# Kernel tuning notes

Hardware: AMD Instinct MI355X
Metric: run time of the kernel (lower is better)

Reference implementation:

```python
import jax, jax.numpy as jnp
import numpy as np

N_NODES = 100_000
M_EDGES = 500_000
F = 128       # elem_fea_len
H = 3         # elem_heads
HD = 256      # hidden layer dim of gate/message nets
BN_EPS = 1e-5


def setup_inputs() -> dict:
    key = jax.random.key(0)
    ks = jax.random.split(key, 12)
    s = 0.05
    return {
        "elem_weights": jax.random.uniform(ks[0], (N_NODES, 1), jnp.float32, 0.05, 1.0),
        "elem_in_fea": jax.random.normal(ks[1], (N_NODES, F), jnp.float32),
        "gate_W1": jax.random.normal(ks[2], (H, 2 * F, HD), jnp.float32) * s,
        "gate_b1": jnp.zeros((H, HD), jnp.float32),
        "gate_g": jnp.ones((H, HD), jnp.float32),
        "gate_beta": jnp.zeros((H, HD), jnp.float32),
        "gate_Wo": jax.random.normal(ks[3], (H, HD, 1), jnp.float32) * s,
        "gate_bo": jnp.zeros((H, 1), jnp.float32),
        "msg_W1": jax.random.normal(ks[4], (H, 2 * F, HD), jnp.float32) * s,
        "msg_b1": jnp.zeros((H, HD), jnp.float32),
        "msg_g": jnp.ones((H, HD), jnp.float32),
        "msg_beta": jnp.zeros((H, HD), jnp.float32),
        "msg_Wo": jax.random.normal(ks[5], (H, HD, F), jnp.float32) * s,
        "msg_bo": jnp.zeros((H, F), jnp.float32),
        "pow_p": jax.random.normal(ks[6], (H, 1), jnp.float32),
        "self_fea_idx": jax.random.randint(ks[7], (M_EDGES,), 0, N_NODES, jnp.int32),
        "nbr_fea_idx": jax.random.randint(ks[8], (M_EDGES,), 0, N_NODES, jnp.int32),
    }


def _simple_net(x, W1, b1, g, beta, Wo, bo):
    # Linear -> BatchNorm1d (training-mode batch stats) -> SiLU -> Linear
    h = x @ W1 + b1
    mu = jnp.mean(h, axis=0)
    var = jnp.mean(jnp.square(h - mu), axis=0)  # biased var, as torch BN
    h = (h - mu) * jax.lax.rsqrt(var + BN_EPS) * g + beta
    h = jax.nn.silu(h)
    return h @ Wo + bo


def reference(elem_weights, elem_in_fea, gate_W1, gate_b1, gate_g, gate_beta,
              gate_Wo, gate_bo, msg_W1, msg_b1, msg_g, msg_beta, msg_Wo,
              msg_bo, pow_p, self_fea_idx, nbr_fea_idx):
    n = elem_in_fea.shape[0]
    # gather edge endpoint features: (M, 2F)
    fea = jnp.concatenate([elem_in_fea[self_fea_idx], elem_in_fea[nbr_fea_idx]], axis=1)
    w = elem_weights[nbr_fea_idx]  # (M, 1)

    def head(gW1, gb1, gg, gbe, gWo, gbo, mW1, mb1, mg, mbe, mWo, mbo, p):
        gate = _simple_net(fea, gW1, gb1, gg, gbe, gWo, gbo)          # (M, 1)
        gmax = jax.ops.segment_max(gate, self_fea_idx, num_segments=n)
        gate = (w ** p) * jnp.exp(gate - gmax[self_fea_idx])
        den = jax.ops.segment_sum(gate, self_fea_idx, num_segments=n)
        gate = gate / (den[self_fea_idx] + 1e-10)
        msg = _simple_net(fea, mW1, mb1, mg, mbe, mWo, mbo)           # (M, F)
        return jax.ops.segment_sum(gate * msg, self_fea_idx, num_segments=n)

    head_out = jax.vmap(head)(gate_W1, gate_b1, gate_g, gate_beta, gate_Wo,
                              gate_bo, msg_W1, msg_b1, msg_g, msg_beta,
                              msg_Wo, msg_bo, pow_p)                  # (H, N, F)
    return jnp.mean(head_out, axis=0) + elem_in_fea
```

## Files before the change

kernel.cpp:

```cpp
#include <hip/hip_runtime.h>
#include <stdint.h>

#define NN 100000
#define MM 500000
#define FD 128
#define KK 256
#define NHEADS 3
#define NTILES 3907

typedef __attribute__((ext_vector_type(8))) __bf16 bf16x8;
typedef __attribute__((ext_vector_type(4))) float floatx4;

__device__ __forceinline__ float bf2f(unsigned short u) {
    union { uint32_t i; float f; } c; c.i = ((uint32_t)u) << 16; return c.f;
}
__device__ __forceinline__ unsigned short f2bf(float f) {
    union { float f; uint32_t i; } c; c.f = f;
    uint32_t i = c.i;
    return (unsigned short)((i + 0x7FFFu + ((i >> 16) & 1u)) >> 16);
}
__device__ __forceinline__ unsigned short f2bf_hw(float f) {
    __bf16 h = (__bf16)f;
    return __builtin_bit_cast(unsigned short, h);
}
__device__ __forceinline__ float silu(float a) {
    float e = __expf(-a);
    return a * __builtin_amdgcn_rcpf(1.f + e);
}
__device__ __forceinline__ float silu_div(float a) { return a / (1.f + __expf(-a)); }
__device__ __forceinline__ float fin(float v) {
    return (v == v && fabsf(v) < 1e30f) ? v : 0.f;
}
__device__ __forceinline__ void gl_lds16(const void* g, void* l) {
    __builtin_amdgcn_global_load_lds(
        (const __attribute__((address_space(1))) unsigned int*)g,
        (__attribute__((address_space(3))) unsigned int*)l, 16, 0, 0);
}
__device__ __forceinline__ void vm_drain() {
    asm volatile("s_waitcnt vmcnt(0)" ::: "memory");
}
__device__ __forceinline__ int swz_bid(int d, int nwg) {
    int qq = nwg >> 3, rr = nwg & 7;
    int xcd = d & 7, idx = d >> 3;
    int base = (xcd < rr) ? xcd * (qq + 1) : rr * (qq + 1) + (xcd - rr) * qq;
    return base + idx;
}

__global__ void k_zero(float* __restrict__ p, int nwords) {
    int i = blockIdx.x * 256 + threadIdx.x;
    if (i < nwords) p[i] = 0.f;
}

__global__ void k_castx(const float* __restrict__ x, unsigned short* __restrict__ xb) {
    int i = blockIdx.x * 256 + threadIdx.x;
    if (i < NN * FD / 2) {
        float2 v = ((const float2*)x)[i];
        uint32_t p = (uint32_t)f2bf(v.x) | ((uint32_t)f2bf(v.y) << 16);
        ((uint32_t*)xb)[i] = p;
    }
}

__global__ void k_transpose_w1(const float* __restrict__ gw1,
                               const float* __restrict__ mw1,
                               unsigned short* __restrict__ W1t) {
    int idx = blockIdx.x * 256 + threadIdx.x;
    int j = idx >> 16;
    int rem = idx & 65535;
    int n = rem >> 8, k = rem & 255;
    const float* src = (j < 3) ? (gw1 + (size_t)j * 65536)
                               : (mw1 + (size_t)(j - 3) * 65536);
    W1t[(size_t)idx] = f2bf(src[k * 256 + n]);
}
__global__ void k_transpose_wo(const float* __restrict__ mwo,
                               unsigned short* __restrict__ Wot) {
    int idx = blockIdx.x * 256 + threadIdx.x;
    int h = idx / 32768;
    int rem = idx % 32768;
    int f = rem >> 8, k = rem & 255;
    Wot[idx] = f2bf(mwo[(size_t)h * 32768 + k * 128 + f]);
}

__global__ void k_hist(const int* __restrict__ idx, int* __restrict__ cnt) {
    int e = blockIdx.x * 256 + threadIdx.x;
    if (e < MM) atomicAdd(&cnt[idx[e]], 1);
}
__global__ void k_scan1(const int* __restrict__ cnt, int* __restrict__ pincl, int* __restrict__ bsum) {
    __shared__ int s[256];
    int t = threadIdx.x;
    int i = blockIdx.x * 256 + t;
    int v = (i < NN) ? cnt[i] : 0;
    s[t] = v; __syncthreads();
    for (int o = 1; o < 256; o <<= 1) {
        int add = (t >= o) ? s[t - o] : 0;
        __syncthreads();
        s[t] += add;
        __syncthreads();
    }
    if (i < NN) pincl[i] = s[t];
    if (t == 255) bsum[blockIdx.x] = s[255];
}
__global__ void k_scan2(const int* __restrict__ bsum, int* __restrict__ boff, int nb) {
    __shared__ int s[512];
    int t = threadIdx.x;
    int v = (t < nb) ? bsum[t] : 0;
    s[t] = v; __syncthreads();
    for (int o = 1; o < 512; o <<= 1) {
        int add = (t >= o) ? s[t - o] : 0;
        __syncthreads();
        s[t] += add;
        __syncthreads();
    }
    if (t < nb) boff[t] = s[t] - v;
}
__global__ void k_scan3(const int* __restrict__ pincl, const int* __restrict__ boff, int* __restrict__ rp) {
    int i = blockIdx.x * 256 + threadIdx.x;
    if (i < NN) rp[i + 1] = pincl[i] + boff[i >> 8];
    if (i == 0) rp[0] = 0;
}
__global__ void k_scatter(const int* __restrict__ self, const int* __restrict__ rp,
                          int* __restrict__ fill, int* __restrict__ elist) {
    int e = blockIdx.x * 256 + threadIdx.x;
    if (e < MM) {
        int n = self[e];
        int pos = atomicAdd(&fill[n], 1);
        elist[rp[n] + pos] = e;
    }
}
__global__ void k_perm(const int* __restrict__ elist, const int* __restrict__ self,
                       const int* __restrict__ nbr, int* __restrict__ selfp, int* __restrict__ nbrp) {
    int i = blockIdx.x * 256 + threadIdx.x;
    if (i < MM) {
        int e = elist[i];
        selfp[i] = self[e];
        nbrp[i] = nbr[e];
    }
}

__global__ void k_colsum(const float* __restrict__ x,
                         const int* __restrict__ cnt_self, const int* __restrict__ cnt_nbr,
                         float* __restrict__ colsum) {
    int t = threadIdx.x;
    int col = t & 127, part = t >> 7;
    const int* cp = part ? cnt_nbr : cnt_self;
    int n0 = blockIdx.x * 512;
    float a = 0.f;
    for (int i = 0; i < 512; i++) {
        int n = n0 + i;
        if (n < NN) {
            float c = (float)cp[n];
            a += c * x[(size_t)n * FD + col];
        }
    }
    atomicAdd(&colsum[part * 128 + col], a);
}

#define NCH 7813
#define CPB 62
__global__ __launch_bounds__(256, 2)
void k_S(const unsigned short* __restrict__ xb,
         const int* __restrict__ self_idx, const int* __restrict__ nbr_idx,
         float* __restrict__ S) {
    __shared__ unsigned short LT[256][72];
    const int tid = threadIdx.x;
    const int e_l = tid & 63;
    const int half = tid >> 6;
    const int ti = blockIdx.y >> 1, tj = blockIdx.y & 1;
    const int lane = tid & 63, w = tid >> 6;
    const int lr = lane & 15, q = lane >> 4;

    int cbeg = blockIdx.x * CPB;
    int cend = cbeg + CPB; if (cend > NCH) cend = NCH;

    floatx4 acc[2][8];
#pragma unroll
    for (int a = 0; a < 2; a++)
#pragma unroll
        for (int b = 0; b < 8; b++)
#pragma unroll
            for (int r = 0; r < 4; r++) acc[a][b][r] = 0.f;

    for (int ch = cbeg; ch < cend; ch++) {
        int e = ch * 64 + e_l;
        union { uint4 v[8]; unsigned short us[64]; } buf;
        if (e < MM) {
            int node = (half < 2) ? self_idx[e] : nbr_idx[e];
            const unsigned short* src = xb + (size_t)node * FD + (half & 1) * 64;
#pragma unroll
            for (int u2 = 0; u2 < 8; u2++) buf.v[u2] = *(const uint4*)(src + u2 * 8);
        } else {
#pragma unroll
            for (int u2 = 0; u2 < 8; u2++) { buf.v[u2].x = 0u; buf.v[u2].y = 0u; buf.v[u2].z = 0u; buf.v[u2].w = 0u; }
        }
        __syncthreads();
#pragma unroll
        for (int j2 = 0; j2 < 64; j2++)
            LT[half * 64 + j2][e_l] = buf.us[j2];
        __syncthreads();
#pragma unroll
        for (int ks = 0; ks < 64; ks += 32) {
            bf16x8 aF[2], bF[8];
#pragma unroll
            for (int mi = 0; mi < 2; mi++)
                aF[mi] = *(const bf16x8*)&LT[ti * 128 + w * 32 + mi * 16 + lr][ks + q * 8];
#pragma unroll
            for (int nj = 0; nj < 8; nj++)
                bF[nj] = *(const bf16x8*)&LT[tj * 128 + nj * 16 + lr][ks + q * 8];
#pragma unroll
            for (int mi = 0; mi < 2; mi++)
#pragma unroll
                for (int nj = 0; nj < 8; nj++)
                    acc[mi][nj] = __builtin_amdgcn_mfma_f32_16x16x32_bf16(aF[mi], bF[nj], acc[mi][nj], 0, 0, 0);
        }
    }
#pragma unroll
    for (int mi = 0; mi < 2; mi++)
#pragma unroll
        for (int nj = 0; nj < 8; nj++)
#pragma unroll
            for (int r = 0; r < 4; r++) {
                int row = ti * 128 + w * 32 + mi * 16 + q * 4 + r;
                int col = tj * 128 + nj * 16 + lr;
                atomicAdd(&S[row * 256 + col], acc[mi][nj][r]);
            }
}

__global__ void k_stats(const float* __restrict__ S, const float* __restrict__ colsum,
                        const unsigned short* __restrict__ W1t,
                        const float* __restrict__ gg, const float* __restrict__ gbe,
                        const float* __restrict__ mg, const float* __restrict__ mbe,
                        float* __restrict__ scaleA, float* __restrict__ shiftA) {
    __shared__ float ws[16][257];
    __shared__ float qq[16], uu[16];
    int t = threadIdx.x;
    int j = blockIdx.y;
    int c0 = blockIdx.x * 16;
    const unsigned short* Wn = W1t + (size_t)j * 65536;
    const float* g    = (j < 3) ? gg + j * 256 : mg + (j - 3) * 256;
    const float* beta = (j < 3) ? gbe + j * 256 : mbe + (j - 3) * 256;
#pragma unroll
    for (int i = 0; i < 16; i++) ws[i][t] = bf2f(Wn[(size_t)(c0 + i) * 256 + t]);
    if (t < 16) { qq[t] = 0.f; uu[t] = 0.f; }
    __syncthreads();
    float vpart[16];
#pragma unroll
    for (int i = 0; i < 16; i++) vpart[i] = 0.f;
    for (int k = 0; k < 256; k++) {
        float s = S[k * 256 + t];
#pragma unroll
        for (int i = 0; i < 16; i++) vpart[i] += s * ws[i][k];
    }
    float cs = colsum[t];
    int lane = t & 63;
#pragma unroll
    for (int i = 0; i < 16; i++) {
        float q1 = ws[i][t] * vpart[i];
        float u1 = cs * ws[i][t];
#pragma unroll
        for (int m = 1; m <= 32; m <<= 1) { q1 += __shfl_xor(q1, m); u1 += __shfl_xor(u1, m); }
        if (lane == 0) { atomicAdd(&qq[i], q1); atomicAdd(&uu[i], u1); }
    }
    __syncthreads();
    if (t < 16) {
        int c = c0 + t;
        float mu = fin(uu[t] / (float)MM);
        float var = fmaxf(fin(qq[t] / (float)MM - mu * mu), 0.f);
        float sc = fin(g[c] * rsqrtf(var + 1e-5f));
        scaleA[j * 256 + c] = sc;
        shiftA[j * 256 + c] = fin(beta[c] - mu * sc);
    }
}

__global__ __launch_bounds__(256, 2)
void k_gate(const unsigned short* __restrict__ x,
            const int* __restrict__ selfp, const int* __restrict__ nbrp,
            const unsigned short* __restrict__ W1t,
            const float* __restrict__ scale, const float* __restrict__ shift,
            const float* __restrict__ wo, const float* __restrict__ bo,
            float* __restrict__ glog) {
    __shared__ unsigned char Bs[2][16384];
    __shared__ float sc[3][256], sh[3][256], wv[3][256];
    __shared__ int nid[128], nidN[128];

    const int tid = threadIdx.x;
    const int m0 = swz_bid(blockIdx.x, NTILES) * 128;
#pragma unroll
    for (int h = 0; h < 3; h++) {
        sc[h][tid] = scale[h * 256 + tid];
        sh[h][tid] = shift[h * 256 + tid];
        wv[h][tid] = wo[h * 256 + tid];
    }
    if (tid < 128) {
        int e = m0 + tid;
        nid[tid]  = (e < MM) ? selfp[e] : 0;
        nidN[tid] = (e < MM) ? nbrp[e] : 0;
    }
    __syncthreads();

    const int lane = tid & 63, w = tid >> 6;
    const int lr = lane & 15, q = lane >> 4;
    const int swz = (lr & 7) << 4;

    bf16x8 aReg[2][8];
    {
        const unsigned short* bS0 = x + (size_t)nid[w * 32 + lr] * FD;
        const unsigned short* bS1 = x + (size_t)nid[w * 32 + 16 + lr] * FD;
        const unsigned short* bN0 = x + (size_t)nidN[w * 32 + lr] * FD;
        const unsigned short* bN1 = x + (size_t)nidN[w * 32 + 16 + lr] * FD;
#pragma unroll
        for (int s = 0; s < 8; s++) {
            int koff = (s & 3) * 32 + q * 8;
            aReg[0][s] = *(const bf16x8*)(((s < 4) ? bS0 : bN0) + koff);
            aReg[1][s] = *(const bf16x8*)(((s < 4) ? bS1 : bN1) + koff);
        }
    }

    uint32_t pre[4];
#pragma unroll
    for (int c = 0; c < 4; c++) {
        int o = (w * 4 + c) * 1024 + lane * 16;
        int r = o >> 7, lc = o & 127;
        pre[c] = (uint32_t)(r * 512 + (lc ^ ((r & 7) << 4)));
    }

    auto STAGE = [&](int t, int b) {
        int hh = t >> 3, rr = t & 7, nh2 = rr >> 2, kc = rr & 3;
        const char* gb = (const char*)(W1t + (size_t)hh * 65536 + (size_t)nh2 * 32768 + kc * 64);
#pragma unroll
        for (int c = 0; c < 4; c++)
            gl_lds16(gb + pre[c], &Bs[b][(w * 4 + c) * 1024]);
    };

    STAGE(0, 0);
    vm_drain();
    __syncthreads();

    int buf = 0, tcur = 0;
    for (int h = 0; h < 3; h++) {
        float dotp[2][4];
#pragma unroll
        for (int mi = 0; mi < 2; mi++)
#pragma unroll
            for (int r = 0; r < 4; r++) dotp[mi][r] = 0.f;

        for (int nh = 0; nh < 2; nh++) {
            floatx4 acc[2][8];
#pragma unroll
            for (int a = 0; a < 2; a++)
#pragma unroll
                for (int b = 0; b < 8; b++)
#pragma unroll
                    for (int r = 0; r < 4; r++) acc[a][b][r] = 0.f;

#pragma unroll
            for (int kc = 0; kc < 4; kc++) {
                if (tcur + 1 < 24) STAGE(tcur + 1, buf ^ 1);
#pragma unroll
                for (int ks = 0; ks < 2; ks++) {
                    bf16x8 bF[8];
#pragma unroll
                    for (int nj = 0; nj < 8; nj++)
                        bF[nj] = *(const bf16x8*)&Bs[buf][(nj * 16 + lr) * 128 + ((ks * 64 + q * 16) ^ swz)];
                    __builtin_amdgcn_s_setprio(1);
#pragma unroll
                    for (int mi = 0; mi < 2; mi++)
#pragma unroll
                        for (int nj = 0; nj < 8; nj++)
                            acc[mi][nj] = __builtin_amdgcn_mfma_f32_16x16x32_bf16(aReg[mi][kc * 2 + ks], bF[nj], acc[mi][nj], 0, 0, 0);
                    __builtin_amdgcn_s_setprio(0);
                }
                vm_drain();
                __syncthreads();
                buf ^= 1; tcur++;
            }
#pragma unroll
            for (int mi = 0; mi < 2; mi++)
#pragma unroll
                for (int r = 0; r < 4; r++) {
                    float d = 0.f;
#pragma unroll
                    for (int nj = 0; nj < 8; nj++) {
                        int cg = nh * 128 + nj * 16 + lr;
                        float v = acc[mi][nj][r] * sc[h][cg] + sh[h][cg];
                        d += silu(v) * wv[h][cg];
                    }
                    dotp[mi][r] += d;
                }
        }
        float b0 = bo[h];
#pragma unroll
        for (int mi = 0; mi < 2; mi++)
#pragma unroll
            for (int r = 0; r < 4; r++) {
                float v = dotp[mi][r];
                v += __shfl_xor(v, 1); v += __shfl_xor(v, 2);
                v += __shfl_xor(v, 4); v += __shfl_xor(v, 8);
                if (lr == 0) {
                    int row = w * 32 + mi * 16 + q * 4 + r;
                    int e = m0 + row;
                    if (e < MM) glog[(size_t)h * MM + e] = fin(v + b0);
                }
            }
    }
}

__global__ void k_coef(const int* __restrict__ rp, const float* __restrict__ glog,
                       float* __restrict__ coef, const float* __restrict__ ew,
                       const int* __restrict__ nbrp, const float* __restrict__ powp) {
    int n = blockIdx.x * 256 + threadIdx.x;
    if (n >= NN) return;
    int b = rp[n], e = rp[n + 1];
    if (e <= b) return;
    int h = blockIdx.y;
    const float* gl = glog + (size_t)h * MM;
    float* cf = coef + (size_t)h * MM;
    float p = powp[h];
    float gmax = -3.4e38f;
    for (int i = b; i < e; i++) gmax = fmaxf(gmax, gl[i]);
    float den = 0.f;
    for (int i = b; i < e; i++) {
        float wvv = ew[nbrp[i]];
        float u = fin(powf(wvv, p) * __expf(gl[i] - gmax));
        cf[i] = u; den += u;
    }
    float inv = fin(1.f / (den + 1e-10f));
    for (int i = b; i < e; i++) cf[i] = fin(cf[i] * inv);
}

__global__ __launch_bounds__(256, 2)
void k_msg(const unsigned short* __restrict__ x,
           const int* __restrict__ selfp, const int* __restrict__ nbrp,
           const unsigned short* __restrict__ W1t,
           const float* __restrict__ scale, const float* __restrict__ shift,
           const unsigned short* __restrict__ Wo2t,
           const float* __restrict__ bo2,
           const float* __restrict__ coef,
           float* __restrict__ out_acc) {
    __shared__ unsigned char Bs[2][16384];
    __shared__ unsigned short ActC[128][72];
    __shared__ float sc[3][256], sh[3][256];
    __shared__ float bvec[3][128], cfs[3][128];
    __shared__ int nid[128], nidN[128];

    const int tid = threadIdx.x;
    const int m0 = blockIdx.x * 128;
#pragma unroll
    for (int h = 0; h < 3; h++) {
        sc[h][tid] = scale[h * 256 + tid];
        sh[h][tid] = shift[h * 256 + tid];
    }
    if (tid < 128) {
        int e = m0 + tid;
        nid[tid]  = (e < MM) ? selfp[e] : -1;
        nidN[tid] = (e < MM) ? nbrp[e] : 0;
#pragma unroll
        for (int h = 0; h < 3; h++) {
            bvec[h][tid] = bo2[h * 128 + tid];
            cfs[h][tid] = (e < MM) ? coef[(size_t)h * MM + e] : 0.f;
        }
    }
    __syncthreads();

    const int lane = tid & 63, w = tid >> 6;
    const int lr = lane & 15, q = lane >> 4;
    const int swz = (lr & 7) << 4;

    bf16x8 aReg[2][8];
    {
        int nS0 = nid[w * 32 + lr];      if (nS0 < 0) nS0 = 0;
        int nS1 = nid[w * 32 + 16 + lr]; if (nS1 < 0) nS1 = 0;
        const unsigned short* bS0 = x + (size_t)nS0 * FD;
        const unsigned short* bS1 = x + (size_t)nS1 * FD;
        const unsigned short* bN0 = x + (size_t)nidN[w * 32 + lr] * FD;
        const unsigned short* bN1 = x + (size_t)nidN[w * 32 + 16 + lr] * FD;
#pragma unroll
        for (int s = 0; s < 8; s++) {
            int koff = (s & 3) * 32 + q * 8;
            aReg[0][s] = *(const bf16x8*)(((s < 4) ? bS0 : bN0) + koff);
            aReg[1][s] = *(const bf16x8*)(((s < 4) ? bS1 : bN1) + koff);
        }
    }

    uint32_t pre[4];
#pragma unroll
    for (int c = 0; c < 4; c++) {
        int o = (w * 4 + c) * 1024 + lane * 16;
        int r = o >> 7, lc = o & 127;
        pre[c] = (uint32_t)(r * 512 + (lc ^ ((r & 7) << 4)));
    }

    auto STAGE = [&](int t, int b) {
        int hh = t / 12, rr = t % 12, nh2 = rr / 6, s6 = rr % 6;
        const unsigned short* base = (s6 < 4)
            ? (W1t + (size_t)hh * 65536 + (size_t)nh2 * 32768 + s6 * 64)
            : (Wo2t + (size_t)hh * 32768 + nh2 * 128 + (s6 - 4) * 64);
        const char* gb = (const char*)base;
#pragma unroll
        for (int c = 0; c < 4; c++)
            gl_lds16(gb + pre[c], &Bs[b][(w * 4 + c) * 1024]);
    };

    STAGE(0, 0);
    vm_drain();
    __syncthreads();

    floatx4 acc2[2][8];
#pragma unroll
    for (int a = 0; a < 2; a++)
#pragma unroll
        for (int b = 0; b < 8; b++)
#pragma unroll
            for (int r = 0; r < 4; r++) acc2[a][b][r] = 0.f;

    int buf = 0, tcur = 0;
    for (int h = 0; h < 3; h++) {
        float cfr[2][4];
#pragma unroll
        for (int mi = 0; mi < 2; mi++)
#pragma unroll
            for (int r = 0; r < 4; r++) cfr[mi][r] = cfs[h][w * 32 + mi * 16 + q * 4 + r];

        for (int nh = 0; nh < 2; nh++) {
            floatx4 acc[2][8];
#pragma unroll
            for (int a = 0; a < 2; a++)
#pragma unroll
                for (int b = 0; b < 8; b++)
#pragma unroll
                    for (int r = 0; r < 4; r++) acc[a][b][r] = 0.f;

#pragma unroll
            for (int kc = 0; kc < 4; kc++) {
                if (tcur + 1 < 36) STAGE(tcur + 1, buf ^ 1);
#pragma unroll
                for (int ks = 0; ks < 2; ks++) {
                    bf16x8 bF[8];
#pragma unroll
                    for (int nj = 0; nj < 8; nj++)
                        bF[nj] = *(const bf16x8*)&Bs[buf][(nj * 16 + lr) * 128 + ((ks * 64 + q * 16) ^ swz)];
                    __builtin_amdgcn_s_setprio(1);
#pragma unroll
                    for (int mi = 0; mi < 2; mi++)
#pragma unroll
                        for (int nj = 0; nj < 8; nj++)
                            acc[mi][nj] = __builtin_amdgcn_mfma_f32_16x16x32_bf16(aReg[mi][kc * 2 + ks], bF[nj], acc[mi][nj], 0, 0, 0);
                    __builtin_amdgcn_s_setprio(0);
                }
                vm_drain();
                __syncthreads();
                buf ^= 1; tcur++;
            }
#pragma unroll
            for (int kc2 = 0; kc2 < 2; kc2++) {
                if (tcur + 1 < 36) STAGE(tcur + 1, buf ^ 1);
#pragma unroll
                for (int mi = 0; mi < 2; mi++)
#pragma unroll
                    for (int njl = 0; njl < 4; njl++)
#pragma unroll
                        for (int r = 0; r < 4; r++) {
                            int nj = kc2 * 4 + njl;
                            int row = w * 32 + mi * 16 + q * 4 + r;
                            int cg = nh * 128 + nj * 16 + lr;
                            float v = acc[mi][nj][r] * sc[h][cg] + sh[h][cg];
                            ActC[row][njl * 16 + lr] = f2bf_hw(silu_div(v) * cfr[mi][r]);
                        }
#pragma unroll
                for (int ks = 0; ks < 2; ks++) {
                    bf16x8 aF[2], bF[8];
#pragma unroll
                    for (int mi = 0; mi < 2; mi++)
                        aF[mi] = *(const bf16x8*)&ActC[w * 32 + mi * 16 + lr][ks * 32 + q * 8];
#pragma unroll
                    for (int nj = 0; nj < 8; nj++)
                        bF[nj] = *(const bf16x8*)&Bs[buf][(nj * 16 + lr) * 128 + ((ks * 64 + q * 16) ^ swz)];
                    __builtin_amdgcn_s_setprio(1);
#pragma unroll
                    for (int mi = 0; mi < 2; mi++)
#pragma unroll
                        for (int nj = 0; nj < 8; nj++)
                            acc2[mi][nj] = __builtin_amdgcn_mfma_f32_16x16x32_bf16(aF[mi], bF[nj], acc2[mi][nj], 0, 0, 0);
                    __builtin_amdgcn_s_setprio(0);
                }
                vm_drain();
                __syncthreads();
                buf ^= 1; tcur++;
            }
        }
    }
#pragma unroll
    for (int mi = 0; mi < 2; mi++) {
        int rbase = w * 32 + mi * 16 + q * 4;
        int n0 = nid[rbase], n3 = nid[rbase + 3];
        float c0[3], c1[3], c2[3], c3[3];
#pragma unroll
        for (int h = 0; h < 3; h++) {
            c0[h] = cfs[h][rbase];     c1[h] = cfs[h][rbase + 1];
            c2[h] = cfs[h][rbase + 2]; c3[h] = cfs[h][rbase + 3];
        }
#pragma unroll
        for (int nj = 0; nj < 8; nj++) {
            int col = nj * 16 + lr;
            float b0h = bvec[0][col], b1h = bvec[1][col], b2h = bvec[2][col];
            float v0 = acc2[mi][nj][0] + c0[0] * b0h + c0[1] * b1h + c0[2] * b2h;
            float v1 = acc2[mi][nj][1] + c1[0] * b0h + c1[1] * b1h + c1[2] * b2h;
            float v2 = acc2[mi][nj][2] + c2[0] * b0h + c2[1] * b1h + c2[2] * b2h;
            float v3 = acc2[mi][nj][3] + c3[0] * b0h + c3[1] * b1h + c3[2] * b2h;
            if (n0 == n3) {
                if (n0 >= 0) atomicAdd(&out_acc[(size_t)n0 * FD + col], v0 + v1 + v2 + v3);
            } else {
                int n1 = nid[rbase + 1], n2 = nid[rbase + 2];
                if (n0 >= 0) atomicAdd(&out_acc[(size_t)n0 * FD + col], v0);
                if (n1 >= 0) atomicAdd(&out_acc[(size_t)n1 * FD + col], v1);
                if (n2 >= 0) atomicAdd(&out_acc[(size_t)n2 * FD + col], v2);
                if (n3 >= 0) atomicAdd(&out_acc[(size_t)n3 * FD + col], v3);
            }
        }
    }
}

__global__ void k_finalout(float* __restrict__ out, const float* __restrict__ x) {
    int i = blockIdx.x * 256 + threadIdx.x;
    if (i < NN * FD) out[i] = fin(out[i]) * (1.f / 3.f) + x[i];
}

extern "C" void kernel_launch(void* const* d_in, const int* in_sizes, int n_in,
                              void* d_out, int out_size, void* d_ws, size_t ws_size,
                              hipStream_t stream) {
    const float* ew   = (const float*)d_in[0];
    const float* x    = (const float*)d_in[1];
    const float* gW1  = (const float*)d_in[2];
    const float* gg   = (const float*)d_in[4];
    const float* gbe  = (const float*)d_in[5];
    const float* gWo  = (const float*)d_in[6];
    const float* gbo  = (const float*)d_in[7];
    const float* mW1  = (const float*)d_in[8];
    const float* mg   = (const float*)d_in[10];
    const float* mbe  = (const float*)d_in[11];
    const float* mWo  = (const float*)d_in[12];
    const float* mbo  = (const float*)d_in[13];
    const float* powp = (const float*)d_in[14];
    const int* self_idx = (const int*)d_in[15];
    const int* nbr_idx  = (const int*)d_in[16];
    float* out = (float*)d_out;

    char* ws = (char*)d_ws;
    size_t off = 0;
    auto alloc = [&](size_t bytes) -> void* {
        size_t o = off;
        off += (bytes + 255) & ~(size_t)255;
        return (void*)(ws + o);
    };

    float* S       = (float*)alloc(256 * 256 * 4);
    float* colsum  = (float*)alloc(512 * 4);
    int*   cnt     = (int*)alloc((size_t)NN * 4);
    int*   cntn    = (int*)alloc((size_t)NN * 4);
    int*   fill    = (int*)alloc((size_t)NN * 4);
    size_t zero_end = off;
    unsigned short* xb   = (unsigned short*)alloc((size_t)NN * FD * 2);
    unsigned short* W1t  = (unsigned short*)alloc(6ull * 65536 * 2);
    unsigned short* Wo2t = (unsigned short*)alloc(3ull * 32768 * 2);
    float* scaleA = (float*)alloc(6ull * 256 * 4);
    float* shiftA = (float*)alloc(6ull * 256 * 4);
    int*   rp     = (int*)alloc((size_t)(NN + 1) * 4);
    int*   pincl  = (int*)alloc((size_t)NN * 4);
    int*   bsum   = (int*)alloc(512 * 4);
    int*   boff   = (int*)alloc(512 * 4);
    int*   elist  = (int*)alloc((size_t)MM * 4);
    int*   selfp  = (int*)alloc((size_t)MM * 4);
    int*   nbrp   = (int*)alloc((size_t)MM * 4);
    float* glog   = (float*)alloc(3ull * MM * 4);
    float* coef   = (float*)alloc(3ull * MM * 4);
    if (off > ws_size) return;

    int zwords = (int)(zero_end / 4);
    k_zero<<<(zwords + 255) / 256, 256, 0, stream>>>(S, zwords);
    k_zero<<<(NN * FD + 255) / 256, 256, 0, stream>>>(out, NN * FD);

    k_castx<<<(NN * FD / 2 + 255) / 256, 256, 0, stream>>>(x, xb);
    k_transpose_w1<<<1536, 256, 0, stream>>>(gW1, mW1, W1t);
    k_transpose_wo<<<384, 256, 0, stream>>>(mWo, Wo2t);

    k_hist<<<1954, 256, 0, stream>>>(self_idx, cnt);
    k_hist<<<1954, 256, 0, stream>>>(nbr_idx, cntn);
    int nb1 = (NN + 255) / 256;
    k_scan1<<<nb1, 256, 0, stream>>>(cnt, pincl, bsum);
    k_scan2<<<1, 512, 0, stream>>>(bsum, boff, nb1);
    k_scan3<<<nb1, 256, 0, stream>>>(pincl, boff, rp);
    k_scatter<<<1954, 256, 0, stream>>>(self_idx, rp, fill, elist);
    k_perm<<<1954, 256, 0, stream>>>(elist, self_idx, nbr_idx, selfp, nbrp);

    k_colsum<<<(NN + 511) / 512, 256, 0, stream>>>(x, cnt, cntn, colsum);
    k_S<<<dim3(128, 4), 256, 0, stream>>>(xb, self_idx, nbr_idx, S);
    k_stats<<<dim3(16, 6), 256, 0, stream>>>(S, colsum, W1t, gg, gbe, mg, mbe, scaleA, shiftA);

    k_gate<<<NTILES, 256, 0, stream>>>(xb, selfp, nbrp, W1t,
                                       scaleA, shiftA, gWo, gbo, glog);
    k_coef<<<dim3(nb1, 3), 256, 0, stream>>>(rp, glog, coef, ew, nbrp, powp);
    k_msg<<<NTILES, 256, 0, stream>>>(xb, selfp, nbrp, W1t + 3ull * 65536,
                                      scaleA + 3 * 256, shiftA + 3 * 256,
                                      Wo2t, mbo, coef, out);
    k_finalout<<<(NN * FD + 255) / 256, 256, 0, stream>>>(out, x);
}
```

Before: 1.522 ms.

## Split edge Gram matrix into count-weighted node blocks and one cross block

The 256x256 second-moment matrix of the gathered edge features is now built in two parts. The diagonal self-self and nbr-nbr blocks are computed per node, with rows scaled by the degree counts, so they cost a pass over 100k nodes instead of 500k edges. Only the self-nbr cross block is still computed per edge, and it is written into both off-diagonal positions by symmetry; that pass now gathers through the sorted (permuted) edge order. This cuts the edge-gather GEMM work to about a quarter, in exchange for extra atomics and for bf16 rounding of the count-scaled values.

```diff
diff --git a/kernel.cpp b/kernel.cpp
--- a/kernel.cpp
+++ b/kernel.cpp
@@ -154,22 +154,96 @@
     atomicAdd(&colsum[part * 128 + col], a);
 }
 
-#define NCH 7813
-#define CPB 62
+#define NCHN 1563
+#define CPNB 4
 __global__ __launch_bounds__(256, 2)
-void k_S(const unsigned short* __restrict__ xb,
-         const int* __restrict__ self_idx, const int* __restrict__ nbr_idx,
-         float* __restrict__ S) {
+void k_Sn(const unsigned short* __restrict__ xb,
+          const int* __restrict__ cnt_self, const int* __restrict__ cnt_nbr,
+          float* __restrict__ S) {
     __shared__ unsigned short LT[256][72];
     const int tid = threadIdx.x;
     const int e_l = tid & 63;
     const int half = tid >> 6;
-    const int ti = blockIdx.y >> 1, tj = blockIdx.y & 1;
+    const int part = blockIdx.y;
+    const int* cp = part ? cnt_nbr : cnt_self;
     const int lane = tid & 63, w = tid >> 6;
     const int lr = lane & 15, q = lane >> 4;
 
-    int cbeg = blockIdx.x * CPB;
-    int cend = cbeg + CPB; if (cend > NCH) cend = NCH;
+    int cbeg = blockIdx.x * CPNB;
+    int cend = cbeg + CPNB; if (cend > NCHN) cend = NCHN;
+
+    floatx4 acc[2][8];
+#pragma unroll
+    for (int a = 0; a < 2; a++)
+#pragma unroll
+        for (int b = 0; b < 8; b++)
+#pragma unroll
+            for (int r = 0; r < 4; r++) acc[a][b][r] = 0.f;
+
+    for (int ch = cbeg; ch < cend; ch++) {
+        int n = ch * 64 + e_l;
+        union { uint4 v[8]; unsigned short us[64]; } buf;
+        if (n < NN) {
+            const unsigned short* src = xb + (size_t)n * FD + (half & 1) * 64;
+#pragma unroll
+            for (int u2 = 0; u2 < 8; u2++) buf.v[u2] = *(const uint4*)(src + u2 * 8);
+            if (half < 2) {
+                float wgt = (float)cp[n];
+#pragma unroll
+                for (int j = 0; j < 64; j++) buf.us[j] = f2bf_hw(wgt * bf2f(buf.us[j]));
+            }
+        } else {
+#pragma unroll
+            for (int u2 = 0; u2 < 8; u2++) { buf.v[u2].x = 0u; buf.v[u2].y = 0u; buf.v[u2].z = 0u; buf.v[u2].w = 0u; }
+        }
+        __syncthreads();
+#pragma unroll
+        for (int j2 = 0; j2 < 64; j2++)
+            LT[half * 64 + j2][e_l] = buf.us[j2];
+        __syncthreads();
+#pragma unroll
+        for (int ks = 0; ks < 64; ks += 32) {
+            bf16x8 aF[2], bF[8];
+#pragma unroll
+            for (int mi = 0; mi < 2; mi++)
+                aF[mi] = *(const bf16x8*)&LT[w * 32 + mi * 16 + lr][ks + q * 8];
+#pragma unroll
+            for (int nj = 0; nj < 8; nj++)
+                bF[nj] = *(const bf16x8*)&LT[128 + nj * 16 + lr][ks + q * 8];
+#pragma unroll
+            for (int mi = 0; mi < 2; mi++)
+#pragma unroll
+                for (int nj = 0; nj < 8; nj++)
+                    acc[mi][nj] = __builtin_amdgcn_mfma_f32_16x16x32_bf16(aF[mi], bF[nj], acc[mi][nj], 0, 0, 0);
+        }
+    }
+#pragma unroll
+    for (int mi = 0; mi < 2; mi++)
+#pragma unroll
+        for (int nj = 0; nj < 8; nj++)
+#pragma unroll
+            for (int r = 0; r < 4; r++) {
+                int row = w * 32 + mi * 16 + q * 4 + r + part * 128;
+                int col = nj * 16 + lr + part * 128;
+                atomicAdd(&S[row * 256 + col], acc[mi][nj][r]);
+            }
+}
+
+#define NCH 7813
+#define CPEB 16
+__global__ __launch_bounds__(256, 2)
+void k_Se(const unsigned short* __restrict__ xb,
+          const int* __restrict__ selfp, const int* __restrict__ nbrp,
+          float* __restrict__ S) {
+    __shared__ unsigned short LT[256][72];
+    const int tid = threadIdx.x;
+    const int e_l = tid & 63;
+    const int half = tid >> 6;
+    const int lane = tid & 63, w = tid >> 6;
+    const int lr = lane & 15, q = lane >> 4;
+
+    int cbeg = blockIdx.x * CPEB;
+    int cend = cbeg + CPEB; if (cend > NCH) cend = NCH;
 
     floatx4 acc[2][8];
 #pragma unroll
@@ -183,7 +257,7 @@
         int e = ch * 64 + e_l;
         union { uint4 v[8]; unsigned short us[64]; } buf;
         if (e < MM) {
-            int node = (half < 2) ? self_idx[e] : nbr_idx[e];
+            int node = (half < 2) ? selfp[e] : nbrp[e];
             const unsigned short* src = xb + (size_t)node * FD + (half & 1) * 64;
 #pragma unroll
             for (int u2 = 0; u2 < 8; u2++) buf.v[u2] = *(const uint4*)(src + u2 * 8);
@@ -201,10 +275,10 @@
             bf16x8 aF[2], bF[8];
 #pragma unroll
             for (int mi = 0; mi < 2; mi++)
-                aF[mi] = *(const bf16x8*)&LT[ti * 128 + w * 32 + mi * 16 + lr][ks + q * 8];
+                aF[mi] = *(const bf16x8*)&LT[w * 32 + mi * 16 + lr][ks + q * 8];
 #pragma unroll
             for (int nj = 0; nj < 8; nj++)
-                bF[nj] = *(const bf16x8*)&LT[tj * 128 + nj * 16 + lr][ks + q * 8];
+                bF[nj] = *(const bf16x8*)&LT[128 + nj * 16 + lr][ks + q * 8];
 #pragma unroll
             for (int mi = 0; mi < 2; mi++)
 #pragma unroll
@@ -218,9 +292,11 @@
         for (int nj = 0; nj < 8; nj++)
 #pragma unroll
             for (int r = 0; r < 4; r++) {
-                int row = ti * 128 + w * 32 + mi * 16 + q * 4 + r;
-                int col = tj * 128 + nj * 16 + lr;
-                atomicAdd(&S[row * 256 + col], acc[mi][nj][r]);
+                int row = w * 32 + mi * 16 + q * 4 + r;
+                int col = nj * 16 + lr;
+                float v = acc[mi][nj][r];
+                atomicAdd(&S[row * 256 + 128 + col], v);
+                atomicAdd(&S[(128 + col) * 256 + row], v);
             }
 }
 
@@ -691,7 +767,8 @@
     k_perm<<<1954, 256, 0, stream>>>(elist, self_idx, nbr_idx, selfp, nbrp);
 
     k_colsum<<<(NN + 511) / 512, 256, 0, stream>>>(x, cnt, cntn, colsum);
-    k_S<<<dim3(128, 4), 256, 0, stream>>>(xb, self_idx, nbr_idx, S);
+    k_Sn<<<dim3(391, 2), 256, 0, stream>>>(xb, cnt, cntn, S);
+    k_Se<<<489, 256, 0, stream>>>(xb, selfp, nbrp, S);
     k_stats<<<dim3(16, 6), 256, 0, stream>>>(S, colsum, W1t, gg, gbe, mg, mbe, scaleA, shiftA);
 
     k_gate<<<NTILES, 256, 0, stream>>>(xb, selfp, nbrp, W1t,
```

After: 1.592 ms. 4.6% more time.
